# Kernel optimization log

Hardware: AMD Instinct MI355X
Metric: run time of the kernel (lower is better)

## Reference

```python
import jax, jax.numpy as jnp
import numpy as np

B, L = 16, 1024
D_MODEL = 384
EXPAND = 2
D_INNER = EXPAND * D_MODEL  # 768
D_STATE = 16
D_CONV = 4
DT_RANK = (D_MODEL + 15) // 16  # 24


def _causal_conv(x, w, b):
    # x: (B,L,Di); w: (Di,K) depthwise kernel; b: (Di,). Causal: pad K-1 on the left.
    K = w.shape[1]
    Lx = x.shape[1]
    xp = jnp.pad(x, ((0, 0), (K - 1, 0), (0, 0)))
    out = sum(xp[:, k:k + Lx, :] * w[:, k] for k in range(K)) + b
    return out


def _selective_scan(u, delta, A, Bm, Cm, Dv):
    # u, delta: (B,L,Di); A: (Di,N); Bm, Cm: (B,L,N); Dv: (Di,)
    def step(h, inp):
        dt, bt, ct, ut = inp  # (B,Di),(B,N),(B,N),(B,Di)
        dA = jnp.exp(dt[..., None] * A)                     # (B,Di,N)
        h = h * dA + (dt * ut)[..., None] * bt[:, None, :]  # (B,Di,N)
        y = jnp.einsum('bdn,bn->bd', h, ct)
        return h, y

    h0 = jnp.zeros((u.shape[0], u.shape[2], A.shape[1]), u.dtype)
    xs = (delta.swapaxes(0, 1), Bm.swapaxes(0, 1), Cm.swapaxes(0, 1), u.swapaxes(0, 1))
    _, ys = jax.lax.scan(step, h0, xs)
    return ys.swapaxes(0, 1) + u * Dv


def _mamba_dir(xz, conv_w, conv_bias, xproj_w, dt_w, dt_b, A_log, Dv):
    xh, z = jnp.split(xz, 2, axis=-1)                 # each (B,L,Di)
    xh = jax.nn.silu(_causal_conv(xh, conv_w, conv_bias))
    dbc = xh @ xproj_w.T                              # (B,L,DT_RANK+2N)
    dt, Bm, Cm = jnp.split(dbc, [DT_RANK, DT_RANK + D_STATE], axis=-1)
    delta = jax.nn.softplus(dt @ dt_w.T + dt_b)       # (B,L,Di)
    A = -jnp.exp(A_log)                               # (Di,N)
    y = _selective_scan(xh, delta, A, Bm, Cm, Dv)
    return y * jax.nn.silu(z)


def setup_inputs():
    key = jax.random.key(0)
    ks = jax.random.split(key, 16)

    def rn(k, shape, s):
        return jax.random.normal(k, shape, dtype=jnp.float32) * s

    A_init = jnp.log(jnp.tile(jnp.arange(1, D_STATE + 1, dtype=jnp.float32), (D_INNER, 1)))
    return dict(
        x=rn(ks[0], (B, L, D_MODEL), 1.0),
        ln_w=jnp.ones((D_MODEL,), jnp.float32),
        ln_b=jnp.zeros((D_MODEL,), jnp.float32),
        in_proj_w=rn(ks[1], (2 * D_INNER, D_MODEL), 0.02),
        out_proj_w=rn(ks[2], (D_MODEL, D_INNER), 0.02),
        conv_w_fwd=rn(ks[3], (D_INNER, D_CONV), 0.2),
        conv_bias_fwd=jnp.zeros((D_INNER,), jnp.float32),
        xproj_w_fwd=rn(ks[4], (DT_RANK + 2 * D_STATE, D_INNER), 0.02),
        dt_w_fwd=rn(ks[5], (D_INNER, DT_RANK), 0.1),
        dt_b_fwd=jnp.full((D_INNER,), -4.0, jnp.float32),
        A_log_fwd=A_init,
        D_fwd=jnp.ones((D_INNER,), jnp.float32),
        conv_w_bwd=rn(ks[6], (D_INNER, D_CONV), 0.2),
        conv_bias_bwd=jnp.zeros((D_INNER,), jnp.float32),
        xproj_w_bwd=rn(ks[7], (DT_RANK + 2 * D_STATE, D_INNER), 0.02),
        dt_w_bwd=rn(ks[8], (D_INNER, DT_RANK), 0.1),
        dt_b_bwd=jnp.full((D_INNER,), -4.0, jnp.float32),
        A_log_bwd=A_init,
        D_bwd=jnp.ones((D_INNER,), jnp.float32),
    )


def reference(x, ln_w, ln_b, in_proj_w, out_proj_w,
              conv_w_fwd, conv_bias_fwd, xproj_w_fwd, dt_w_fwd, dt_b_fwd, A_log_fwd, D_fwd,
              conv_w_bwd, conv_bias_bwd, xproj_w_bwd, dt_w_bwd, dt_b_bwd, A_log_bwd, D_bwd):
    # LayerNorm
    mu = x.mean(-1, keepdims=True)
    var = ((x - mu) ** 2).mean(-1, keepdims=True)
    xn = (x - mu) / jnp.sqrt(var + 1e-5) * ln_w + ln_b
    # Shared input projection -> (B,L,2*Di)
    xz = xn @ in_proj_w.T
    # Forward-direction mamba branch
    out_f = _mamba_dir(xz, conv_w_fwd, conv_bias_fwd, xproj_w_fwd, dt_w_fwd, dt_b_fwd, A_log_fwd, D_fwd)
    # Backward-direction branch on sequence-flipped xz, flipped back (bimamba v2)
    out_r = _mamba_dir(xz[:, ::-1], conv_w_bwd, conv_bias_bwd, xproj_w_bwd, dt_w_bwd, dt_b_bwd, A_log_bwd, D_bwd)[:, ::-1]
    # Output projection + residual (drop_path=0 -> identity)
    return x + (out_f + out_r) @ out_proj_w.T
```

## Files before the change

### kernel.cpp

```cpp
#include <hip/hip_runtime.h>
#include <cstdint>
#include <cstddef>

#define BN_   16
#define LN_   1024
#define DM_   384
#define DI_   768
#define NS_   16
#define RDT_  24
#define NDBC_ 56
#define NDBCP 64
#define NC_   16
#define LC_   64

typedef unsigned short ushortT;
typedef short bf16x8 __attribute__((ext_vector_type(8)));
typedef float f32x4 __attribute__((ext_vector_type(4)));

typedef __attribute__((address_space(3))) uint32_t lds_u32_t;
typedef __attribute__((address_space(1))) const uint32_t glb_u32_t;

static __device__ __forceinline__ void stage16(const void* g, void* lds) {
    __builtin_amdgcn_global_load_lds(
        (glb_u32_t*)(uintptr_t)g,
        (lds_u32_t*)(uint32_t)(uintptr_t)lds,
        16, 0, 0);
}

static __device__ __forceinline__ float silu_f(float x) {
    return x / (1.0f + __expf(-x));
}
static __device__ __forceinline__ float softplus_f(float s) {
    return fmaxf(s, 0.0f) + __logf(1.0f + __expf(-fabsf(s)));
}
static __device__ __forceinline__ ushortT f2bf(float f) {
    union { float f; uint32_t u; } v; v.f = f;
    uint32_t u = v.u;
    uint32_t r = u + 0x7fffu + ((u >> 16) & 1u);
    return (ushortT)(r >> 16);
}
static __device__ __forceinline__ float bf2f(ushortT b) {
    union { uint32_t u; float f; } v; v.u = ((uint32_t)b) << 16;
    return v.f;
}

__global__ __launch_bounds__(256) void wconv_kernel(
    const float* __restrict__ w1, int n1, const float* __restrict__ w2, int n2,
    const float* __restrict__ xwf, const float* __restrict__ xwb,
    const float* __restrict__ dwf, const float* __restrict__ dwb,
    ushortT* __restrict__ o1, ushortT* __restrict__ o2,
    ushortT* __restrict__ oxf, ushortT* __restrict__ oxb,
    ushortT* __restrict__ odf, ushortT* __restrict__ odb)
{
    int i = blockIdx.x * 256 + threadIdx.x;
    if (i < n1) { o1[i] = f2bf(w1[i]); return; }
    i -= n1;
    if (i < n2) { o2[i] = f2bf(w2[i]); return; }
    i -= n2;
    const int nx = NDBCP * DI_;
    if (i < 2 * nx) {
        int which = i >= nx;
        int j = which ? (i - nx) : i;
        int row = j / DI_;
        const float* src = which ? xwb : xwf;
        ushortT* dst = which ? oxb : oxf;
        dst[j] = (row < NDBC_) ? f2bf(src[j]) : (ushortT)0;
        return;
    }
    i -= 2 * nx;
    const int nd = DI_ * 32;
    if (i < 2 * nd) {
        int which = i >= nd;
        int j = which ? (i - nd) : i;
        int row = j >> 5, col = j & 31;
        const float* src = which ? dwb : dwf;
        ushortT* dst = which ? odb : odf;
        dst[j] = (col < RDT_) ? f2bf(src[row * RDT_ + col]) : (ushortT)0;
    }
}

__global__ __launch_bounds__(256) void ln_kernel(
    const float* __restrict__ x, const float* __restrict__ w,
    const float* __restrict__ b, ushortT* __restrict__ xn,
    int row0, int nrows)
{
    int r = blockIdx.x * 4 + (threadIdx.x >> 6);
    if (r >= nrows) return;
    int lane = threadIdx.x & 63;
    const float* xr = x + (size_t)(row0 + r) * DM_;
    float v[6];
    float s = 0.0f;
#pragma unroll
    for (int i = 0; i < 6; i++) { v[i] = xr[lane + 64 * i]; s += v[i]; }
#pragma unroll
    for (int o = 32; o > 0; o >>= 1) s += __shfl_down(s, o, 64);
    s = __shfl(s, 0, 64);
    float mu = s * (1.0f / DM_);
    float q = 0.0f;
#pragma unroll
    for (int i = 0; i < 6; i++) { float d = v[i] - mu; q += d * d; }
#pragma unroll
    for (int o = 32; o > 0; o >>= 1) q += __shfl_down(q, o, 64);
    q = __shfl(q, 0, 64);
    float rstd = rsqrtf(q * (1.0f / DM_) + 1e-5f);
    ushortT* outp = xn + (size_t)r * DM_;
#pragma unroll
    for (int i = 0; i < 6; i++) {
        int c = lane + 64 * i;
        outp[c] = f2bf((v[i] - mu) * rstd * w[c] + b[c]);
    }
}

template <int BM, int BN, int WR, int WC, bool CAT, bool RES, bool OB>
__global__ __launch_bounds__(256) void gemm_mfma(
    const ushortT* __restrict__ Aa, const ushortT* __restrict__ Ab_,
    const ushortT* __restrict__ W, const float* __restrict__ R,
    void* __restrict__ Cv, int M, int N, int Khalf)
{
    constexpr int WTM = BM / WR;
    constexpr int WTN = BN / WC;
    constexpr int FM = WTM / 16;
    constexpr int FN = WTN / 16;
    __shared__ ushortT As[BM * 32];
    __shared__ ushortT Ws[BN * 32];
    int tid = threadIdx.x;
    int bm = blockIdx.x * BM, bn = blockIdx.y * BN;
    int wave = tid >> 6, lane = tid & 63;
    int wm = wave % WR, wn = wave / WR;
    f32x4 acc[FM][FN] = {};
    int Ktot = CAT ? 2 * Khalf : Khalf;
    int lrow = lane >> 2;
    int lk = (lane & 3) * 8;

    for (int k0 = 0; k0 < Ktot; k0 += 32) {
        const ushortT* Asrc = (!CAT || k0 < Khalf) ? Aa : Ab_;
        int ka = (!CAT || k0 < Khalf) ? k0 : (k0 - Khalf);
        __syncthreads();
#pragma unroll
        for (int c = 0; c < BM / 64; c++) {
            int ch = c * 4 + wave;
            int row = ch * 16 + lrow;
            stage16(Asrc + (size_t)(bm + row) * Khalf + ka + lk, &As[ch * 16 * 32]);
        }
#pragma unroll
        for (int c = 0; c < BN / 64; c++) {
            int ch = c * 4 + wave;
            int row = ch * 16 + lrow;
            stage16(W + (size_t)(bn + row) * Khalf + ka + lk, &Ws[ch * 16 * 32]);
        }
        __syncthreads();
        int mb = (wm * WTM + (lane & 15)) * 32 + (lane >> 4) * 8;
        int nb = (wn * WTN + (lane & 15)) * 32 + (lane >> 4) * 8;
        bf16x8 af[FM], bfr[FN];
#pragma unroll
        for (int mi = 0; mi < FM; mi++) af[mi] = *(bf16x8*)&As[mb + mi * 16 * 32];
#pragma unroll
        for (int ni = 0; ni < FN; ni++) bfr[ni] = *(bf16x8*)&Ws[nb + ni * 16 * 32];
#pragma unroll
        for (int mi = 0; mi < FM; mi++)
#pragma unroll
            for (int ni = 0; ni < FN; ni++)
                acc[mi][ni] = __builtin_amdgcn_mfma_f32_16x16x32_bf16(
                    af[mi], bfr[ni], acc[mi][ni], 0, 0, 0);
    }

#pragma unroll
    for (int mi = 0; mi < FM; mi++) {
        int row = bm + wm * WTM + 16 * mi + (lane >> 4) * 4;
#pragma unroll
        for (int ni = 0; ni < FN; ni++) {
            int col = bn + wn * WTN + 16 * ni + (lane & 15);
#pragma unroll
            for (int r = 0; r < 4; r++) {
                size_t o = (size_t)(row + r) * N + col;
                float v = acc[mi][ni][r];
                if (RES) v += R[o];
                if (OB) ((ushortT*)Cv)[o] = f2bf(v);
                else    ((float*)Cv)[o] = v;
            }
        }
    }
}

__global__ __launch_bounds__(256) void conv_kernel(
    const ushortT* __restrict__ XZ,
    const float* __restrict__ wf, const float* __restrict__ bf,
    const float* __restrict__ wb, const float* __restrict__ bb,
    ushortT* __restrict__ XH, int gB)
{
    const int D8 = DI_ / 8;
    int idx = blockIdx.x * 256 + threadIdx.x;
    int perdir = gB * LN_ * D8;
    int dir = 0;
    if (idx >= perdir) { idx -= perdir; dir = 1; }
    int d8 = idx % D8;
    int l = (idx / D8) & (LN_ - 1);
    int b = idx / (D8 * LN_);
    int d = d8 * 8;
    const float* cw = (dir ? wb : wf) + d * 4;
    const float* cb = (dir ? bb : bf) + d;

    float xv[4][8];
#pragma unroll
    for (int k = 0; k < 4; k++) {
        int j = l - 3 + k;
        if (j < 0) {
#pragma unroll
            for (int c = 0; c < 8; c++) xv[k][c] = 0.0f;
        } else {
            int ls = dir ? (LN_ - 1 - j) : j;
            ushort4 v = *(const ushort4*)(XZ + (size_t)(b * LN_ + ls) * (2 * DI_) + d);
            ushort4 v2 = *(const ushort4*)(XZ + (size_t)(b * LN_ + ls) * (2 * DI_) + d + 4);
            xv[k][0] = bf2f(v.x);  xv[k][1] = bf2f(v.y);
            xv[k][2] = bf2f(v.z);  xv[k][3] = bf2f(v.w);
            xv[k][4] = bf2f(v2.x); xv[k][5] = bf2f(v2.y);
            xv[k][6] = bf2f(v2.z); xv[k][7] = bf2f(v2.w);
        }
    }
    ushortT out[8];
#pragma unroll
    for (int c = 0; c < 8; c++) {
        float4 w4 = *(const float4*)(cw + c * 4);
        float s = cb[c];
        s = fmaf(xv[0][c], w4.x, s);
        s = fmaf(xv[1][c], w4.y, s);
        s = fmaf(xv[2][c], w4.z, s);
        s = fmaf(xv[3][c], w4.w, s);
        out[c] = f2bf(silu_f(s));
    }
    ushortT* op = XH + ((size_t)dir * gB * LN_ + (size_t)(b * LN_ + l)) * DI_ + d;
    *(ushort4*)(op + 0) = make_ushort4(out[0], out[1], out[2], out[3]);
    *(ushort4*)(op + 4) = make_ushort4(out[4], out[5], out[6], out[7]);
}

__global__ __launch_bounds__(256) void xproj_mfma(
    const ushortT* __restrict__ XH, const ushortT* __restrict__ Wf,
    const ushortT* __restrict__ Wb, float* __restrict__ Cf,
    float* __restrict__ Cb, ushortT* __restrict__ DT24, int mblocksPerDir)
{
    __shared__ ushortT As[64 * 32];
    __shared__ ushortT Ws[64 * 32];
    int blk = blockIdx.x;
    int dir = blk >= mblocksPerDir;
    const ushortT* W = dir ? Wb : Wf;
    float* C = dir ? Cb : Cf;
    int bmG = blk * 64;
    int bmC = (blk - dir * mblocksPerDir) * 64;
    int tid = threadIdx.x, wave = tid >> 6, lane = tid & 63;
    f32x4 acc[4] = {};
    int lrow = lane >> 2;
    int lk = (lane & 3) * 8;

    for (int k0 = 0; k0 < DI_; k0 += 32) {
        __syncthreads();
        stage16(XH + (size_t)(bmG + wave * 16 + lrow) * DI_ + k0 + lk, &As[wave * 16 * 32]);
        stage16(W + (size_t)(wave * 16 + lrow) * DI_ + k0 + lk, &Ws[wave * 16 * 32]);
        __syncthreads();
        bf16x8 bfr = *(bf16x8*)&Ws[(wave * 16 + (lane & 15)) * 32 + (lane >> 4) * 8];
#pragma unroll
        for (int mi = 0; mi < 4; mi++) {
            bf16x8 af = *(bf16x8*)&As[(mi * 16 + (lane & 15)) * 32 + (lane >> 4) * 8];
            acc[mi] = __builtin_amdgcn_mfma_f32_16x16x32_bf16(af, bfr, acc[mi], 0, 0, 0);
        }
    }
#pragma unroll
    for (int mi = 0; mi < 4; mi++) {
        int row = bmC + 16 * mi + (lane >> 4) * 4;
        int col = wave * 16 + (lane & 15);
#pragma unroll
        for (int r = 0; r < 4; r++)
            C[(size_t)(row + r) * NDBCP + col] = acc[mi][r];
    }
    if (wave < 2) {
        ushortT* dtp = DT24 + (size_t)dir * (size_t)(mblocksPerDir * 64) * 32;
        int col = wave * 16 + (lane & 15);
#pragma unroll
        for (int mi = 0; mi < 4; mi++) {
            int row = bmC + 16 * mi + (lane >> 4) * 4;
#pragma unroll
            for (int r = 0; r < 4; r++)
                dtp[(size_t)(row + r) * 32 + col] =
                    (col < RDT_) ? f2bf(acc[mi][r]) : (ushortT)0;
        }
    }
}

__global__ __launch_bounds__(256) void dtud_kernel(
    const ushortT* __restrict__ DT24, const ushortT* __restrict__ WDtf,
    const ushortT* __restrict__ WDtb,
    const float* __restrict__ dtbf, const float* __restrict__ dtbb,
    const ushortT* __restrict__ XH, uint32_t* __restrict__ UD, int rows)
{
    __shared__ ushortT As[128 * 32];
    __shared__ ushortT Ws[64 * 32];
    int dir = blockIdx.z;
    int bm = blockIdx.x * 128;
    int bn = blockIdx.y * 64;
    const ushortT* A = DT24 + (size_t)dir * rows * 32;
    const ushortT* W = dir ? WDtb : WDtf;
    const float* dtb = dir ? dtbb : dtbf;
    const ushortT* xh = XH + (size_t)dir * rows * DI_;
    uint32_t* ud = UD + (size_t)dir * rows * DI_;
    int tid = threadIdx.x, wave = tid >> 6, lane = tid & 63;
    int lrow = lane >> 2, lk = (lane & 3) * 8;

    stage16(A + (size_t)(bm + wave * 16 + lrow) * 32 + lk, &As[wave * 16 * 32]);
    stage16(A + (size_t)(bm + 64 + wave * 16 + lrow) * 32 + lk, &As[(64 + wave * 16) * 32]);
    stage16(W + (size_t)(bn + wave * 16 + lrow) * 32 + lk, &Ws[wave * 16 * 32]);
    __syncthreads();

    f32x4 acc[2][4] = {};
    bf16x8 bfr[4];
#pragma unroll
    for (int ni = 0; ni < 4; ni++)
        bfr[ni] = *(bf16x8*)&Ws[(ni * 16 + (lane & 15)) * 32 + (lane >> 4) * 8];
#pragma unroll
    for (int mi = 0; mi < 2; mi++) {
        bf16x8 af = *(bf16x8*)&As[(wave * 32 + mi * 16 + (lane & 15)) * 32 + (lane >> 4) * 8];
#pragma unroll
        for (int ni = 0; ni < 4; ni++)
            acc[mi][ni] = __builtin_amdgcn_mfma_f32_16x16x32_bf16(
                af, bfr[ni], acc[mi][ni], 0, 0, 0);
    }
#pragma unroll
    for (int ni = 0; ni < 4; ni++) {
        int d = bn + ni * 16 + (lane & 15);
        float bias = dtb[d];
#pragma unroll
        for (int mi = 0; mi < 2; mi++) {
            int rb = bm + wave * 32 + mi * 16 + (lane >> 4) * 4;
#pragma unroll
            for (int r = 0; r < 4; r++) {
                int row = rb + r;
                float dt = softplus_f(acc[mi][ni][r] + bias);
                float u = bf2f(xh[(size_t)row * DI_ + d]);
                ud[(size_t)row * DI_ + d] =
                    ((uint32_t)f2bf(dt) << 16) | (uint32_t)f2bf(u);
            }
        }
    }
}

__global__ __launch_bounds__(256) void scan1_kernel(
    const uint32_t* __restrict__ UD,
    const float* __restrict__ dbcf, const float* __restrict__ dbcb,
    const float* __restrict__ alogf, const float* __restrict__ alogb,
    float* __restrict__ hs1, float* __restrict__ dec, int gB)
{
    int bid = blockIdx.x;
    int c = bid % NC_; bid /= NC_;
    int dchunk = bid % 3; bid /= 3;
    int b = bid % gB;
    int dir = bid / gB;
    int d = dchunk * 256 + threadIdx.x;

    const float* dbc  = dir ? dbcb : dbcf;
    const float* alog = dir ? alogb : alogf;

    float An[NS_];
#pragma unroll
    for (int n = 0; n < NS_; n++) An[n] = -__expf(alog[d * NS_ + n]);
    float a1 = An[0];
    bool pk = true;
#pragma unroll
    for (int n = 0; n < NS_; n++)
        pk = pk && (fabsf(An[n] - (float)(n + 1) * a1) <=
                    1e-3f * (float)(n + 1) * fabsf(a1) + 1e-6f);
    pk = (bool)__all((int)pk);

    __shared__ float sB[LC_ * 16];
    int rb = b * LN_ + c * LC_;
    int jb = c * LC_;
    {
        int row = threadIdx.x >> 2, c4 = (threadIdx.x & 3) * 4;
        *(float4*)&sB[row * 16 + c4] =
            *(const float4*)(dbc + (size_t)(rb + row) * NDBCP + RDT_ + c4);
    }
    __syncthreads();

    float h[NS_];
#pragma unroll
    for (int n = 0; n < NS_; n++) h[n] = 0.0f;
    float S = 0.0f;
    const uint32_t* udp = UD + (size_t)((dir * gB + b) * LN_ + jb) * DI_ + d;

    if (pk) {
        for (int lt = 0; lt < LC_; lt += 8) {
            uint32_t ud8[8];
#pragma unroll
            for (int i = 0; i < 8; i++) ud8[i] = udp[(lt + i) * DI_];
#pragma unroll
            for (int i = 0; i < 8; i++) {
                int lr = lt + i;
                const float4* Bp4 = (const float4*)&sB[lr * 16];
                float4 B0 = Bp4[0], B1 = Bp4[1], B2 = Bp4[2], B3 = Bp4[3];
                float Bv[NS_] = {B0.x, B0.y, B0.z, B0.w, B1.x, B1.y, B1.z, B1.w,
                                 B2.x, B2.y, B2.z, B2.w, B3.x, B3.y, B3.z, B3.w};
                float u = bf2f((ushortT)(ud8[i] & 0xffffu));
                float dt = bf2f((ushortT)(ud8[i] >> 16));
                S += dt;
                float du = dt * u;
                float q1 = __expf(dt * a1);
                float q2 = q1 * q1, q4 = q2 * q2, q8 = q4 * q4;
                float p2 = q2, p3 = q2 * q1, p5 = q4 * q1, p6 = q4 * q2, p7 = q4 * p3;
                float pw[NS_] = {q1, p2, p3, q4, p5, p6, p7, q8,
                                 q8 * q1, q8 * p2, q8 * p3, q8 * q4,
                                 q8 * p5, q8 * p6, q8 * p7, q8 * q8};
#pragma unroll
                for (int n = 0; n < NS_; n++)
                    h[n] = fmaf(h[n], pw[n], du * Bv[n]);
            }
        }
        float q1 = __expf(S * a1);
        float q2 = q1 * q1, q4 = q2 * q2, q8 = q4 * q4;
        float p2 = q2, p3 = q2 * q1, p5 = q4 * q1, p6 = q4 * q2, p7 = q4 * p3;
        float pw[NS_] = {q1, p2, p3, q4, p5, p6, p7, q8,
                         q8 * q1, q8 * p2, q8 * p3, q8 * q4,
                         q8 * p5, q8 * p6, q8 * p7, q8 * q8};
        int si = (((dir * gB + b) * NC_ + c) * DI_ + d) * NS_;
#pragma unroll
        for (int n = 0; n < NS_; n++) {
            hs1[si + n] = h[n];
            dec[si + n] = pw[n];
        }
    } else {
        for (int lr = 0; lr < LC_; lr++) {
            const float* rowp = &sB[lr * 16];
            uint32_t udv = udp[lr * DI_];
            float u = bf2f((ushortT)(udv & 0xffffu));
            float dt = bf2f((ushortT)(udv >> 16));
            S += dt;
            float du = dt * u;
#pragma unroll
            for (int n = 0; n < NS_; n++)
                h[n] = fmaf(h[n], __expf(dt * An[n]), du * rowp[n]);
        }
        int si = (((dir * gB + b) * NC_ + c) * DI_ + d) * NS_;
#pragma unroll
        for (int n = 0; n < NS_; n++) {
            hs1[si + n] = h[n];
            dec[si + n] = __expf(An[n] * S);
        }
    }
}

__global__ __launch_bounds__(256) void scan2_kernel(
    const float* __restrict__ hs1, const float* __restrict__ dec,
    float* __restrict__ hin, int gB)
{
    int e = blockIdx.x * 256 + threadIdx.x;
    int n = e & 15; int e2 = e >> 4;
    int d = e2 % DI_; e2 /= DI_;
    int b = e2 % gB; int dir = e2 / gB;
    int base = (((dir * gB + b) * NC_) * DI_ + d) * NS_ + n;
    float h = 0.0f;
    const int cs = DI_ * NS_;
    for (int c = 0; c < NC_; c++) {
        int idx = base + c * cs;
        hin[idx] = h;
        h = fmaf(h, dec[idx], hs1[idx]);
    }
}

__global__ __launch_bounds__(256) void scan3_kernel(
    const uint32_t* __restrict__ UD, const ushortT* __restrict__ XZ,
    const float* __restrict__ dbcf, const float* __restrict__ dbcb,
    const float* __restrict__ alogf, const float* __restrict__ dvf,
    const float* __restrict__ alogb, const float* __restrict__ dvb,
    const float* __restrict__ hin,
    ushortT* __restrict__ yf, ushortT* __restrict__ yb, int gB)
{
    int bid = blockIdx.x;
    int c = bid % NC_; bid /= NC_;
    int dchunk = bid % 3; bid /= 3;
    int b = bid % gB;
    int dir = bid / gB;
    int d = dchunk * 256 + threadIdx.x;

    const float* dbc  = dir ? dbcb : dbcf;
    const float* alog = dir ? alogb : alogf;
    float Dd          = (dir ? dvb : dvf)[d];
    ushortT* y        = dir ? yb : yf;

    float An[NS_];
#pragma unroll
    for (int n = 0; n < NS_; n++) An[n] = -__expf(alog[d * NS_ + n]);
    float a1 = An[0];
    bool pk = true;
#pragma unroll
    for (int n = 0; n < NS_; n++)
        pk = pk && (fabsf(An[n] - (float)(n + 1) * a1) <=
                    1e-3f * (float)(n + 1) * fabsf(a1) + 1e-6f);
    pk = (bool)__all((int)pk);

    __shared__ float sBC[LC_ * 32];
    int rb = b * LN_ + c * LC_;
    int jb = c * LC_;
#pragma unroll
    for (int i = 0; i < 2; i++) {
        int idx = threadIdx.x + 256 * i;
        int row = idx >> 3, c4 = (idx & 7) * 4;
        *(float4*)&sBC[row * 32 + c4] =
            *(const float4*)(dbc + (size_t)(rb + row) * NDBCP + RDT_ + c4);
    }
    __syncthreads();

    int si = (((dir * gB + b) * NC_ + c) * DI_ + d) * NS_;
    float h[NS_];
#pragma unroll
    for (int n = 0; n < NS_; n++) h[n] = hin[si + n];
    const uint32_t* udp = UD + (size_t)((dir * gB + b) * LN_ + jb) * DI_ + d;

    if (pk) {
        for (int lt = 0; lt < LC_; lt += 8) {
            uint32_t ud8[8];
            ushortT z8[8];
#pragma unroll
            for (int i = 0; i < 8; i++) {
                ud8[i] = udp[(lt + i) * DI_];
                int j = jb + lt + i;
                int lo = dir ? (LN_ - 1 - j) : j;
                z8[i] = XZ[(size_t)(b * LN_ + lo) * (2 * DI_) + DI_ + d];
            }
#pragma unroll
            for (int i = 0; i < 8; i++) {
                int lr = lt + i;
                const float4* rp4 = (const float4*)&sBC[lr * 32];
                float4 B0 = rp4[0], B1 = rp4[1], B2 = rp4[2], B3 = rp4[3];
                float4 C0 = rp4[4], C1 = rp4[5], C2 = rp4[6], C3 = rp4[7];
                float Bv[NS_] = {B0.x, B0.y, B0.z, B0.w, B1.x, B1.y, B1.z, B1.w,
                                 B2.x, B2.y, B2.z, B2.w, B3.x, B3.y, B3.z, B3.w};
                float Cw[NS_] = {C0.x, C0.y, C0.z, C0.w, C1.x, C1.y, C1.z, C1.w,
                                 C2.x, C2.y, C2.z, C2.w, C3.x, C3.y, C3.z, C3.w};
                float u = bf2f((ushortT)(ud8[i] & 0xffffu));
                float dt = bf2f((ushortT)(ud8[i] >> 16));
                float du = dt * u;
                float q1 = __expf(dt * a1);
                float q2 = q1 * q1, q4 = q2 * q2, q8 = q4 * q4;
                float p2 = q2, p3 = q2 * q1, p5 = q4 * q1, p6 = q4 * q2, p7 = q4 * p3;
                float pw[NS_] = {q1, p2, p3, q4, p5, p6, p7, q8,
                                 q8 * q1, q8 * p2, q8 * p3, q8 * q4,
                                 q8 * p5, q8 * p6, q8 * p7, q8 * q8};
                float y0 = 0.f, y1 = 0.f, y2 = 0.f, y3 = 0.f;
#pragma unroll
                for (int n = 0; n < NS_; n += 4) {
                    h[n + 0] = fmaf(h[n + 0], pw[n + 0], du * Bv[n + 0]);
                    h[n + 1] = fmaf(h[n + 1], pw[n + 1], du * Bv[n + 1]);
                    h[n + 2] = fmaf(h[n + 2], pw[n + 2], du * Bv[n + 2]);
                    h[n + 3] = fmaf(h[n + 3], pw[n + 3], du * Bv[n + 3]);
                    y0 = fmaf(h[n + 0], Cw[n + 0], y0);
                    y1 = fmaf(h[n + 1], Cw[n + 1], y1);
                    y2 = fmaf(h[n + 2], Cw[n + 2], y2);
                    y3 = fmaf(h[n + 3], Cw[n + 3], y3);
                }
                float yv = ((y0 + y1) + (y2 + y3)) + u * Dd;
                int j = jb + lr;
                int lo = dir ? (LN_ - 1 - j) : j;
                float z = bf2f(z8[i]);
                y[(b * LN_ + lo) * DI_ + d] = f2bf(yv * silu_f(z));
            }
        }
    } else {
        for (int lr = 0; lr < LC_; lr++) {
            const float* rowp = &sBC[lr * 32];
            uint32_t ud = udp[lr * DI_];
            float u = bf2f((ushortT)(ud & 0xffffu));
            float dt = bf2f((ushortT)(ud >> 16));
            float du = dt * u;
            float y0 = 0.f, y1 = 0.f, y2 = 0.f, y3 = 0.f;
#pragma unroll
            for (int n = 0; n < NS_; n += 4) {
                h[n + 0] = fmaf(h[n + 0], __expf(dt * An[n + 0]), du * rowp[n + 0]);
                h[n + 1] = fmaf(h[n + 1], __expf(dt * An[n + 1]), du * rowp[n + 1]);
                h[n + 2] = fmaf(h[n + 2], __expf(dt * An[n + 2]), du * rowp[n + 2]);
                h[n + 3] = fmaf(h[n + 3], __expf(dt * An[n + 3]), du * rowp[n + 3]);
                y0 = fmaf(h[n + 0], rowp[16 + n + 0], y0);
                y1 = fmaf(h[n + 1], rowp[16 + n + 1], y1);
                y2 = fmaf(h[n + 2], rowp[16 + n + 2], y2);
                y3 = fmaf(h[n + 3], rowp[16 + n + 3], y3);
            }
            float yv = ((y0 + y1) + (y2 + y3)) + u * Dd;
            int j = jb + lr;
            int lo = dir ? (LN_ - 1 - j) : j;
            float z = bf2f(XZ[(size_t)(b * LN_ + lo) * (2 * DI_) + DI_ + d]);
            y[(b * LN_ + lo) * DI_ + d] = f2bf(yv * silu_f(z));
        }
    }
}

extern "C" void kernel_launch(void* const* d_in, const int* in_sizes, int n_in,
                              void* d_out, int out_size, void* d_ws, size_t ws_size,
                              hipStream_t stream)
{
    const float* x         = (const float*)d_in[0];
    const float* ln_w      = (const float*)d_in[1];
    const float* ln_b      = (const float*)d_in[2];
    const float* in_proj_w = (const float*)d_in[3];
    const float* out_proj_w= (const float*)d_in[4];
    const float* conv_wf   = (const float*)d_in[5];
    const float* conv_bf   = (const float*)d_in[6];
    const float* xproj_f   = (const float*)d_in[7];
    const float* dt_wf     = (const float*)d_in[8];
    const float* dt_bf     = (const float*)d_in[9];
    const float* alog_f    = (const float*)d_in[10];
    const float* dv_f      = (const float*)d_in[11];
    const float* conv_wb   = (const float*)d_in[12];
    const float* conv_bb   = (const float*)d_in[13];
    const float* xproj_b   = (const float*)d_in[14];
    const float* dt_wb     = (const float*)d_in[15];
    const float* dt_bb     = (const float*)d_in[16];
    const float* alog_b    = (const float*)d_in[17];
    const float* dv_b      = (const float*)d_in[18];
    float* outp = (float*)d_out;

    const int n_w1 = 2 * DI_ * DM_;
    const int n_w2 = DM_ * DI_;
    const int n_wx = NDBCP * DI_;
    const int n_wd = DI_ * 32;

    uint8_t* base = (uint8_t*)d_ws;
    size_t off = 0;
    auto alloc = [&](size_t nbytes) {
        uint8_t* r = base + off;
        off = (off + nbytes + 255) & ~(size_t)255;
        return r;
    };
    ushortT* WbIn  = (ushortT*)alloc((size_t)n_w1 * 2);
    ushortT* WbOut = (ushortT*)alloc((size_t)n_w2 * 2);
    ushortT* WbXf  = (ushortT*)alloc((size_t)n_wx * 2);
    ushortT* WbXb  = (ushortT*)alloc((size_t)n_wx * 2);
    ushortT* WbDtf = (ushortT*)alloc((size_t)n_wd * 2);
    ushortT* WbDtb = (ushortT*)alloc((size_t)n_wd * 2);
    size_t fixed_bytes = off;

    size_t per_b_bytes = 24ull * 1024 * 1024;
    int g = BN_;
    while (g > 1 && fixed_bytes + (size_t)g * per_b_bytes + (1ull << 20) > ws_size) g >>= 1;

    wconv_kernel<<<(n_w1 + n_w2 + 2 * n_wx + 2 * n_wd + 255) / 256, 256, 0, stream>>>(
        in_proj_w, n_w1, out_proj_w, n_w2, xproj_f, xproj_b, dt_wf, dt_wb,
        WbIn, WbOut, WbXf, WbXb, WbDtf, WbDtb);

    for (int b0 = 0; b0 < BN_; b0 += g) {
        int rows = g * LN_;
        off = fixed_bytes;
        ushortT* XNb  = (ushortT*)alloc((size_t)rows * DM_ * 2);
        ushortT* XZ   = (ushortT*)alloc((size_t)rows * 2 * DI_ * 2);
        ushortT* XH   = (ushortT*)alloc((size_t)2 * rows * DI_ * 2);
        float* DBCf   = (float*)alloc((size_t)rows * NDBCP * 4);
        float* DBCb   = (float*)alloc((size_t)rows * NDBCP * 4);
        ushortT* DT24 = (ushortT*)alloc((size_t)2 * rows * 32 * 2);
        uint32_t* UD  = (uint32_t*)alloc((size_t)2 * rows * DI_ * 4);
        size_t st_n   = (size_t)2 * g * NC_ * DI_ * NS_;
        float* HS1    = (float*)alloc(st_n * 4);
        float* DEC    = (float*)alloc(st_n * 4);
        float* HIN    = (float*)alloc(st_n * 4);
        ushortT* Yf   = (ushortT*)alloc((size_t)rows * DI_ * 2);
        ushortT* Yb   = (ushortT*)alloc((size_t)rows * DI_ * 2);
        int row0 = b0 * LN_;

        ln_kernel<<<rows / 4, 256, 0, stream>>>(x, ln_w, ln_b, XNb, row0, rows);

        gemm_mfma<128, 128, 2, 2, false, false, true>
            <<<dim3(rows / 128, (2 * DI_) / 128), 256, 0, stream>>>(
            XNb, nullptr, WbIn, nullptr, XZ, rows, 2 * DI_, DM_);

        conv_kernel<<<(2 * rows * (DI_ / 8)) / 256, 256, 0, stream>>>(
            XZ, conv_wf, conv_bf, conv_wb, conv_bb, XH, g);

        xproj_mfma<<<2 * (rows / 64), 256, 0, stream>>>(
            XH, WbXf, WbXb, DBCf, DBCb, DT24, rows / 64);

        dtud_kernel<<<dim3(rows / 128, DI_ / 64, 2), 256, 0, stream>>>(
            DT24, WbDtf, WbDtb, dt_bf, dt_bb, XH, UD, rows);

        scan1_kernel<<<2 * g * 3 * NC_, 256, 0, stream>>>(
            UD, DBCf, DBCb, alog_f, alog_b, HS1, DEC, g);

        scan2_kernel<<<(2 * g * DI_ * NS_) / 256, 256, 0, stream>>>(HS1, DEC, HIN, g);

        scan3_kernel<<<2 * g * 3 * NC_, 256, 0, stream>>>(
            UD, XZ, DBCf, DBCb, alog_f, dv_f, alog_b, dv_b,
            HIN, Yf, Yb, g);

        gemm_mfma<64, 128, 1, 4, true, true, false>
            <<<dim3(rows / 64, DM_ / 128), 256, 0, stream>>>(
            Yf, Yb, WbOut, x + (size_t)row0 * DM_,
            outp + (size_t)row0 * DM_, rows, DM_, DI_);
    }
}
```

Before: 511.8 us.

## Pack chunk scan states to bf16 and prefetch next tile of scan inputs

Scan1 now writes each chunk-end state and its decay factor as one packed pair of bf16 values instead of two fp32 arrays. Scan2 reads the packed pair and writes the carried-in state as bf16, which cuts the memory traffic of the inter-chunk pass. Scan1 and scan3 also double-buffer their loads of dt/u (and z in scan3), fetching the next group of eight rows while computing on the current one. The bf16 state storage loses precision in the carried hidden state, and the smaller workspace per batch may let more batches be processed per pass.

```diff
diff --git a/kernel.cpp b/kernel.cpp
--- a/kernel.cpp
+++ b/kernel.cpp
@@ -345,7 +345,7 @@
     const uint32_t* __restrict__ UD,
     const float* __restrict__ dbcf, const float* __restrict__ dbcb,
     const float* __restrict__ alogf, const float* __restrict__ alogb,
-    float* __restrict__ hs1, float* __restrict__ dec, int gB)
+    uint32_t* __restrict__ SD, int gB)
 {
     int bid = blockIdx.x;
     int c = bid % NC_; bid /= NC_;
@@ -385,10 +385,17 @@
     const uint32_t* udp = UD + (size_t)((dir * gB + b) * LN_ + jb) * DI_ + d;
 
     if (pk) {
+        uint32_t ud8[8];
+#pragma unroll
+        for (int i = 0; i < 8; i++) ud8[i] = udp[i * DI_];
         for (int lt = 0; lt < LC_; lt += 8) {
-            uint32_t ud8[8];
-#pragma unroll
-            for (int i = 0; i < 8; i++) ud8[i] = udp[(lt + i) * DI_];
+            uint32_t cur[8];
+#pragma unroll
+            for (int i = 0; i < 8; i++) cur[i] = ud8[i];
+            if (lt + 8 < LC_) {
+#pragma unroll
+                for (int i = 0; i < 8; i++) ud8[i] = udp[(lt + 8 + i) * DI_];
+            }
 #pragma unroll
             for (int i = 0; i < 8; i++) {
                 int lr = lt + i;
@@ -396,8 +403,8 @@
                 float4 B0 = Bp4[0], B1 = Bp4[1], B2 = Bp4[2], B3 = Bp4[3];
                 float Bv[NS_] = {B0.x, B0.y, B0.z, B0.w, B1.x, B1.y, B1.z, B1.w,
                                  B2.x, B2.y, B2.z, B2.w, B3.x, B3.y, B3.z, B3.w};
-                float u = bf2f((ushortT)(ud8[i] & 0xffffu));
-                float dt = bf2f((ushortT)(ud8[i] >> 16));
+                float u = bf2f((ushortT)(cur[i] & 0xffffu));
+                float dt = bf2f((ushortT)(cur[i] >> 16));
                 S += dt;
                 float du = dt * u;
                 float q1 = __expf(dt * a1);
@@ -419,10 +426,8 @@
                          q8 * p5, q8 * p6, q8 * p7, q8 * q8};
         int si = (((dir * gB + b) * NC_ + c) * DI_ + d) * NS_;
 #pragma unroll
-        for (int n = 0; n < NS_; n++) {
-            hs1[si + n] = h[n];
-            dec[si + n] = pw[n];
-        }
+        for (int n = 0; n < NS_; n++)
+            SD[si + n] = ((uint32_t)f2bf(pw[n]) << 16) | (uint32_t)f2bf(h[n]);
     } else {
         for (int lr = 0; lr < LC_; lr++) {
             const float* rowp = &sB[lr * 16];
@@ -437,16 +442,14 @@
         }
         int si = (((dir * gB + b) * NC_ + c) * DI_ + d) * NS_;
 #pragma unroll
-        for (int n = 0; n < NS_; n++) {
-            hs1[si + n] = h[n];
-            dec[si + n] = __expf(An[n] * S);
-        }
+        for (int n = 0; n < NS_; n++)
+            SD[si + n] = ((uint32_t)f2bf(__expf(An[n] * S)) << 16) |
+                         (uint32_t)f2bf(h[n]);
     }
 }
 
 __global__ __launch_bounds__(256) void scan2_kernel(
-    const float* __restrict__ hs1, const float* __restrict__ dec,
-    float* __restrict__ hin, int gB)
+    const uint32_t* __restrict__ SD, ushortT* __restrict__ hin, int gB)
 {
     int e = blockIdx.x * 256 + threadIdx.x;
     int n = e & 15; int e2 = e >> 4;
@@ -457,8 +460,9 @@
     const int cs = DI_ * NS_;
     for (int c = 0; c < NC_; c++) {
         int idx = base + c * cs;
-        hin[idx] = h;
-        h = fmaf(h, dec[idx], hs1[idx]);
+        uint32_t sd = SD[idx];
+        hin[idx] = f2bf(h);
+        h = fmaf(h, bf2f((ushortT)(sd >> 16)), bf2f((ushortT)(sd & 0xffffu)));
     }
 }
 
@@ -467,7 +471,7 @@
     const float* __restrict__ dbcf, const float* __restrict__ dbcb,
     const float* __restrict__ alogf, const float* __restrict__ dvf,
     const float* __restrict__ alogb, const float* __restrict__ dvb,
-    const float* __restrict__ hin,
+    const ushortT* __restrict__ hin,
     ushortT* __restrict__ yf, ushortT* __restrict__ yb, int gB)
 {
     int bid = blockIdx.x;
@@ -508,19 +512,32 @@
     int si = (((dir * gB + b) * NC_ + c) * DI_ + d) * NS_;
     float h[NS_];
 #pragma unroll
-    for (int n = 0; n < NS_; n++) h[n] = hin[si + n];
+    for (int n = 0; n < NS_; n++) h[n] = bf2f(hin[si + n]);
     const uint32_t* udp = UD + (size_t)((dir * gB + b) * LN_ + jb) * DI_ + d;
 
     if (pk) {
+        uint32_t ud8[8];
+        ushortT z8[8];
+#pragma unroll
+        for (int i = 0; i < 8; i++) {
+            ud8[i] = udp[i * DI_];
+            int j = jb + i;
+            int lo = dir ? (LN_ - 1 - j) : j;
+            z8[i] = XZ[(size_t)(b * LN_ + lo) * (2 * DI_) + DI_ + d];
+        }
         for (int lt = 0; lt < LC_; lt += 8) {
-            uint32_t ud8[8];
-            ushortT z8[8];
-#pragma unroll
-            for (int i = 0; i < 8; i++) {
-                ud8[i] = udp[(lt + i) * DI_];
-                int j = jb + lt + i;
-                int lo = dir ? (LN_ - 1 - j) : j;
-                z8[i] = XZ[(size_t)(b * LN_ + lo) * (2 * DI_) + DI_ + d];
+            uint32_t cud[8];
+            ushortT cz[8];
+#pragma unroll
+            for (int i = 0; i < 8; i++) { cud[i] = ud8[i]; cz[i] = z8[i]; }
+            if (lt + 8 < LC_) {
+#pragma unroll
+                for (int i = 0; i < 8; i++) {
+                    ud8[i] = udp[(lt + 8 + i) * DI_];
+                    int j = jb + lt + 8 + i;
+                    int lo = dir ? (LN_ - 1 - j) : j;
+                    z8[i] = XZ[(size_t)(b * LN_ + lo) * (2 * DI_) + DI_ + d];
+                }
             }
 #pragma unroll
             for (int i = 0; i < 8; i++) {
@@ -532,8 +549,8 @@
                                  B2.x, B2.y, B2.z, B2.w, B3.x, B3.y, B3.z, B3.w};
                 float Cw[NS_] = {C0.x, C0.y, C0.z, C0.w, C1.x, C1.y, C1.z, C1.w,
                                  C2.x, C2.y, C2.z, C2.w, C3.x, C3.y, C3.z, C3.w};
-                float u = bf2f((ushortT)(ud8[i] & 0xffffu));
-                float dt = bf2f((ushortT)(ud8[i] >> 16));
+                float u = bf2f((ushortT)(cud[i] & 0xffffu));
+                float dt = bf2f((ushortT)(cud[i] >> 16));
                 float du = dt * u;
                 float q1 = __expf(dt * a1);
                 float q2 = q1 * q1, q4 = q2 * q2, q8 = q4 * q4;
@@ -556,7 +573,7 @@
                 float yv = ((y0 + y1) + (y2 + y3)) + u * Dd;
                 int j = jb + lr;
                 int lo = dir ? (LN_ - 1 - j) : j;
-                float z = bf2f(z8[i]);
+                float z = bf2f(cz[i]);
                 y[(b * LN_ + lo) * DI_ + d] = f2bf(yv * silu_f(z));
             }
         }
@@ -633,7 +650,7 @@
     ushortT* WbDtb = (ushortT*)alloc((size_t)n_wd * 2);
     size_t fixed_bytes = off;
 
-    size_t per_b_bytes = 24ull * 1024 * 1024;
+    size_t per_b_bytes = 21ull * 1024 * 1024;
     int g = BN_;
     while (g > 1 && fixed_bytes + (size_t)g * per_b_bytes + (1ull << 20) > ws_size) g >>= 1;
 
@@ -652,9 +669,8 @@
         ushortT* DT24 = (ushortT*)alloc((size_t)2 * rows * 32 * 2);
         uint32_t* UD  = (uint32_t*)alloc((size_t)2 * rows * DI_ * 4);
         size_t st_n   = (size_t)2 * g * NC_ * DI_ * NS_;
-        float* HS1    = (float*)alloc(st_n * 4);
-        float* DEC    = (float*)alloc(st_n * 4);
-        float* HIN    = (float*)alloc(st_n * 4);
+        uint32_t* SD  = (uint32_t*)alloc(st_n * 4);
+        ushortT* HIN  = (ushortT*)alloc(st_n * 2);
         ushortT* Yf   = (ushortT*)alloc((size_t)rows * DI_ * 2);
         ushortT* Yb   = (ushortT*)alloc((size_t)rows * DI_ * 2);
         int row0 = b0 * LN_;
@@ -675,9 +691,9 @@
             DT24, WbDtf, WbDtb, dt_bf, dt_bb, XH, UD, rows);
 
         scan1_kernel<<<2 * g * 3 * NC_, 256, 0, stream>>>(
-            UD, DBCf, DBCb, alog_f, alog_b, HS1, DEC, g);
-
-        scan2_kernel<<<(2 * g * DI_ * NS_) / 256, 256, 0, stream>>>(HS1, DEC, HIN, g);
+            UD, DBCf, DBCb, alog_f, alog_b, SD, g);
+
+        scan2_kernel<<<(2 * g * DI_ * NS_) / 256, 256, 0, stream>>>(SD, HIN, g);
 
         scan3_kernel<<<2 * g * 3 * NC_, 256, 0, stream>>>(
             UD, XZ, DBCf, DBCb, alog_f, dv_f, alog_b, dv_b,
```

Result: faster. 486.2 us (-5.0%).
